# Optimization experiments

Hardware: AMD Instinct MI355X
Metric: run time of the kernel (lower is better)

The kernel has to match this reference:

```python
import jax, jax.numpy as jnp
import numpy as np

N_NODES = 50000
N_EDGES = 600000
D_FEAT = 128
HIDDEN = 128
N_CLASSES = 47


def setup_inputs() -> dict:
    key = jax.random.key(0)
    ks = jax.random.split(key, 8)
    x = jax.random.normal(ks[0], (N_NODES, D_FEAT), dtype=jnp.float32)
    edge_index = jax.random.randint(ks[1], (2, N_EDGES), 0, N_NODES, dtype=jnp.int64)
    def glorot(k, shape):
        fan_in, fan_out = shape
        s = jnp.sqrt(2.0 / (fan_in + fan_out)).astype(jnp.float32)
        return jax.random.normal(k, shape, dtype=jnp.float32) * s
    return {
        "x": x,
        "edge_index": edge_index,
        "Wl0": glorot(ks[2], (D_FEAT, HIDDEN)),
        "bl0": jnp.zeros((HIDDEN,), jnp.float32),
        "Wr0": glorot(ks[3], (D_FEAT, HIDDEN)),
        "Wl1": glorot(ks[4], (HIDDEN, HIDDEN)),
        "bl1": jnp.zeros((HIDDEN,), jnp.float32),
        "Wr1": glorot(ks[5], (HIDDEN, HIDDEN)),
        "Wl2": glorot(ks[6], (HIDDEN, N_CLASSES)),
        "bl2": jnp.zeros((N_CLASSES,), jnp.float32),
        "Wr2": glorot(ks[7], (HIDDEN, N_CLASSES)),
    }


def _sage_conv(x, src, dst, Wl, bl, Wr, n_nodes):
    # mean-aggregate neighbor (source) features at destination nodes
    msg = x[src]                                                  # [E, D] gather
    agg = jax.ops.segment_sum(msg, dst, num_segments=n_nodes)     # [N, D]
    deg = jax.ops.segment_sum(jnp.ones((src.shape[0],), x.dtype), dst,
                              num_segments=n_nodes)               # [N]
    agg = agg / jnp.maximum(deg, 1.0)[:, None]
    # PyG SAGEConv: lin_l(aggr) + lin_r(x_root); bias lives in lin_l
    return agg @ Wl + bl + x @ Wr


def reference(x, edge_index, Wl0, bl0, Wr0, Wl1, bl1, Wr1, Wl2, bl2, Wr2):
    src, dst = edge_index[0], edge_index[1]
    n = x.shape[0]
    h = jax.nn.relu(_sage_conv(x, src, dst, Wl0, bl0, Wr0, n))
    h = jax.nn.relu(_sage_conv(h, src, dst, Wl1, bl1, Wr1, n))
    h = _sage_conv(h, src, dst, Wl2, bl2, Wr2, n)
    # F.normalize(p=2, dim=-1): eps-clamped L2 norm (torch eps=1e-12)
    norm = jnp.maximum(jnp.linalg.norm(h, axis=-1, keepdims=True), 1e-12)
    h = h / norm
    return jax.nn.log_softmax(h, axis=1)
```

## Files before the change

kernel.cpp:

```cpp
#include <hip/hip_runtime.h>
#include <stdint.h>

#define N_NODES 50000
#define N_EDGES 600000
#define NCLS    47
#define SCAN_TPB 512
#define SCAN_BLOCKS ((N_NODES + SCAN_TPB - 1) / SCAN_TPB)

typedef __attribute__((ext_vector_type(8))) short short8;
typedef __attribute__((ext_vector_type(4))) float f32x4;

static __device__ __forceinline__ float bf2f(uint16_t h) {
    union { uint32_t u; float f; } c; c.u = ((uint32_t)h) << 16; return c.f;
}
static __device__ __forceinline__ float bf2fs(short h) { return bf2f((uint16_t)h); }
static __device__ __forceinline__ uint16_t f2bf(float f) {
    union { float f; uint32_t u; } c; c.f = f;
    uint32_t u = c.u;
    return (uint16_t)((u + 0x7fffu + ((u >> 16) & 1u)) >> 16);
}

__global__ __launch_bounds__(256) void k_split(const float4* __restrict__ x,
                                               ushort4* __restrict__ xh) {
    int i = blockIdx.x * 256 + threadIdx.x;
    float4 v = x[i];
    ushort4 h;
    h.x = f2bf(v.x);
    h.y = f2bf(v.y);
    h.z = f2bf(v.z);
    h.w = f2bf(v.w);
    xh[i] = h;
}

__global__ __launch_bounds__(256) void k_deg(const int* __restrict__ ei,
                                             int* __restrict__ deg) {
    __shared__ int is64;
    {
        int lane = threadIdx.x;
        if (lane < 64) {
            int f = ei[2 * lane + 1] | ei[2 * lane + 129];
            unsigned long long m = __ballot(f != 0);
            if (lane == 0) is64 = (m == 0ULL) ? 1 : 0;
        }
        __syncthreads();
    }
    int e = blockIdx.x * 256 + threadIdx.x;
    if (e < N_EDGES) {
        int d = is64 ? ei[2 * (N_EDGES + e)] : ei[N_EDGES + e];
        d = min(max(d, 0), N_NODES - 1);
        atomicAdd(&deg[d], 1);
    }
}

__global__ __launch_bounds__(SCAN_TPB) void k_scan1(const int* __restrict__ deg,
                                                    int* __restrict__ partial) {
    int t = blockIdx.x * SCAN_TPB + threadIdx.x;
    int v = (t < N_NODES) ? deg[t] : 0;
#pragma unroll
    for (int o = 1; o < 64; o <<= 1) v += __shfl_xor(v, o);
    __shared__ int ws[SCAN_TPB / 64];
    int lane = threadIdx.x & 63, w = threadIdx.x >> 6;
    if (lane == 0) ws[w] = v;
    __syncthreads();
    if (threadIdx.x == 0) {
        int s = 0;
#pragma unroll
        for (int i = 0; i < SCAN_TPB / 64; ++i) s += ws[i];
        partial[blockIdx.x] = s;
    }
}

__global__ __launch_bounds__(128) void k_scan2(int* __restrict__ partial) {
    __shared__ int sh[128];
    int t = threadIdx.x;
    int v = (t < SCAN_BLOCKS) ? partial[t] : 0;
    sh[t] = v;
    __syncthreads();
    for (int o = 1; o < 128; o <<= 1) {
        int u = (t >= o) ? sh[t - o] : 0;
        __syncthreads();
        sh[t] += u;
        __syncthreads();
    }
    if (t < SCAN_BLOCKS) partial[t] = sh[t] - v;
}

__global__ __launch_bounds__(SCAN_TPB) void k_scan3(const int* __restrict__ deg,
                                                    const int* __restrict__ partial,
                                                    int* __restrict__ row_start,
                                                    int* __restrict__ fill,
                                                    float* __restrict__ inv_deg) {
    int tb = threadIdx.x;
    int t = blockIdx.x * SCAN_TPB + tb;
    int v = (t < N_NODES) ? deg[t] : 0;
    int lane = tb & 63, w = tb >> 6;
    int inc = v;
#pragma unroll
    for (int o = 1; o < 64; o <<= 1) {
        int u = __shfl_up(inc, o);
        if (lane >= o) inc += u;
    }
    __shared__ int wsum[SCAN_TPB / 64];
    if (lane == 63) wsum[w] = inc;
    __syncthreads();
    int woff = 0;
    for (int i = 0; i < w; ++i) woff += wsum[i];
    int excl = partial[blockIdx.x] + woff + (inc - v);
    if (t < N_NODES) {
        row_start[t] = excl;
        fill[t] = excl;
        inv_deg[t] = 1.0f / (float)(v > 0 ? v : 1);
    }
}

__global__ __launch_bounds__(256) void k_fill(const int* __restrict__ ei,
                                              int* __restrict__ fill,
                                              int* __restrict__ elist) {
    __shared__ int is64;
    {
        int lane = threadIdx.x;
        if (lane < 64) {
            int f = ei[2 * lane + 1] | ei[2 * lane + 129];
            unsigned long long m = __ballot(f != 0);
            if (lane == 0) is64 = (m == 0ULL) ? 1 : 0;
        }
        __syncthreads();
    }
    int e = blockIdx.x * 256 + threadIdx.x;
    if (e < N_EDGES) {
        int s, d;
        if (is64) { s = ei[2 * e]; d = ei[2 * (N_EDGES + e)]; }
        else      { s = ei[e];     d = ei[N_EDGES + e]; }
        s = min(max(s, 0), N_NODES - 1);
        d = min(max(d, 0), N_NODES - 1);
        int pos = atomicAdd(&fill[d], 1);
        elist[pos] = s;
    }
}

__global__ __launch_bounds__(256) void k_agg(const uint16_t* __restrict__ hm_h,
                                             const int* __restrict__ row_start,
                                             const int* __restrict__ degv,
                                             const float* __restrict__ inv_deg,
                                             const int* __restrict__ elist,
                                             uint16_t* __restrict__ agg_h) {
    int lane = threadIdx.x & 63;
    int node = blockIdx.x * 4 + (threadIdx.x >> 6);
    if (node >= N_NODES) return;
    int g = lane >> 4;
    int li = lane & 15;
    int j = li * 8;
    int rs = row_start[node];
    int d = degv[node];
    float a[8];
#pragma unroll
    for (int k = 0; k < 8; ++k) a[k] = 0.f;
    int i = g;
    for (; i + 4 < d; i += 8) {
        int s0 = elist[rs + i];
        int s1 = elist[rs + i + 4];
        short8 w0 = *(const short8*)&hm_h[(size_t)s0 * 128 + j];
        short8 w1 = *(const short8*)&hm_h[(size_t)s1 * 128 + j];
#pragma unroll
        for (int k = 0; k < 8; ++k) a[k] += bf2fs(w0[k]) + bf2fs(w1[k]);
    }
    if (i < d) {
        int s = elist[rs + i];
        short8 w = *(const short8*)&hm_h[(size_t)s * 128 + j];
#pragma unroll
        for (int k = 0; k < 8; ++k) a[k] += bf2fs(w[k]);
    }
    float sc = inv_deg[node];
    short8 oh;
#pragma unroll
    for (int k = 0; k < 8; ++k) {
        float v = a[k];
        v += __shfl_xor(v, 16);
        v += __shfl_xor(v, 32);
        oh[k] = (short)f2bf(v * sc);
    }
    if (g == 0) *(short8*)&agg_h[(size_t)node * 128 + j] = oh;
}

__global__ __launch_bounds__(256) void k_prepw(const float* Wl0, const float* Wr0,
                                               const float* Wl1, const float* Wr1,
                                               const float* Wl2, const float* Wr2,
                                               uint16_t* __restrict__ img) {
    int b = blockIdx.x >> 6;
    int sub = blockIdx.x & 63;
    const float* W; int ncol, npad; uint16_t* o;
    switch (b) {
        case 0: W = Wl0; ncol = 128; npad = 128; o = img;           break;
        case 1: W = Wr0; ncol = 128; npad = 128; o = img + 32768;   break;
        case 2: W = Wl1; ncol = 128; npad = 128; o = img + 65536;   break;
        case 3: W = Wr1; ncol = 128; npad = 128; o = img + 98304;   break;
        case 4: W = Wl2; ncol = 47;  npad = 48;  o = img + 131072;  break;
        default:W = Wr2; ncol = 47;  npad = 48;  o = img + 143360;  break;
    }
    int elems = npad * 128;
    int i = sub * 256 + threadIdx.x;
    if (i < elems) {
        int col = i % npad, k = i / npad;
        float v = (col < ncol) ? W[k * ncol + col] : 0.f;
        uint16_t h = f2bf(v);
        uint16_t l = f2bf(v - bf2f(h));
        int idx = col * 128 + (((k >> 3) ^ (col & 15)) << 3) + (k & 7);
        o[idx] = h;
        o[idx + elems] = l;
    }
}

__global__ __launch_bounds__(512) void k_gemm(const uint16_t* __restrict__ A1h,
                                              const uint16_t* __restrict__ A2h,
                                              const uint16_t* __restrict__ wl,
                                              const uint16_t* __restrict__ wr,
                                              const float* __restrict__ bias,
                                              uint16_t* __restrict__ outh) {
    __shared__ __align__(16) uint16_t ldsW[32768];
    int tid = threadIdx.x;
    int lane = tid & 63, wv = tid >> 6;
    int li = lane & 15, g4 = lane >> 4;
    int mrow = blockIdx.x * 128 + wv * 16 + li;
    int r0 = min(mrow, N_NODES - 1);

    f32x4 acc[8];
#pragma unroll
    for (int t = 0; t < 8; ++t) acc[t] = (f32x4){0.f, 0.f, 0.f, 0.f};

#pragma unroll
    for (int arr = 0; arr < 2; ++arr) {
        {
            const uint4* g = (const uint4*)(arr ? wr : wl);
            uint4* l = (uint4*)ldsW;
#pragma unroll
            for (int j2 = 0; j2 < 8; ++j2)
                l[j2 * 512 + tid] = g[j2 * 512 + tid];
        }
        __syncthreads();

        const uint16_t* Ah = arr ? A2h : A1h;
#pragma unroll
        for (int s = 0; s < 4; ++s) {
            int ko = s * 32 + g4 * 8;
            short8 a0h = *(const short8*)&Ah[(size_t)r0 * 128 + ko];
#pragma unroll
            for (int t = 0; t < 8; ++t) {
                int off = (t * 16 + li) * 128 + (((s * 4 + g4) ^ li) << 3);
                short8 bh = *(const short8*)&ldsW[off];
                short8 bl = *(const short8*)&ldsW[off + 16384];
                acc[t] = __builtin_amdgcn_mfma_f32_16x16x32_bf16(a0h, bh, acc[t], 0, 0, 0);
                acc[t] = __builtin_amdgcn_mfma_f32_16x16x32_bf16(a0h, bl, acc[t], 0, 0, 0);
            }
        }
        if (arr == 0) __syncthreads();
    }
    int rowbase = blockIdx.x * 128 + wv * 16 + g4 * 4;
#pragma unroll
    for (int t = 0; t < 8; ++t) {
        int col = t * 16 + li;
        float bv = bias[col];
#pragma unroll
        for (int rr = 0; rr < 4; ++rr) {
            int row = rowbase + rr;
            if (row < N_NODES)
                outh[(size_t)row * 128 + col] = f2bf(fmaxf(acc[t][rr] + bv, 0.f));
        }
    }
}

__global__ __launch_bounds__(512) void k_gemm2(const uint16_t* __restrict__ A1h,
                                               const uint16_t* __restrict__ A2h,
                                               const uint16_t* __restrict__ w2,
                                               const float* __restrict__ bias,
                                               float* __restrict__ out) {
    __shared__ __align__(16) uint16_t ldsW[24576];
    int tid = threadIdx.x;
    int lane = tid & 63, wv = tid >> 6;
    int li = lane & 15, g4 = lane >> 4;
    int mrow = blockIdx.x * 128 + wv * 16 + li;
    int r = min(mrow, N_NODES - 1);

    {
        const uint4* g = (const uint4*)w2;
        uint4* l = (uint4*)ldsW;
#pragma unroll
        for (int j2 = 0; j2 < 12; ++j2)
            l[j2 * 512 + tid] = g[j2 * 512 + tid];
    }
    __syncthreads();

    f32x4 acc[3];
#pragma unroll
    for (int t = 0; t < 3; ++t) acc[t] = (f32x4){0.f, 0.f, 0.f, 0.f};

#pragma unroll
    for (int arr = 0; arr < 2; ++arr) {
        const uint16_t* Ah = arr ? A2h : A1h;
        const uint16_t* WL = &ldsW[arr * 12288];
#pragma unroll
        for (int s = 0; s < 4; ++s) {
            int ko = s * 32 + g4 * 8;
            short8 ah = *(const short8*)&Ah[(size_t)r * 128 + ko];
#pragma unroll
            for (int t = 0; t < 3; ++t) {
                int off = (t * 16 + li) * 128 + (((s * 4 + g4) ^ li) << 3);
                short8 bh = *(const short8*)&WL[off];
                short8 bl = *(const short8*)&WL[off + 6144];
                acc[t] = __builtin_amdgcn_mfma_f32_16x16x32_bf16(ah, bh, acc[t], 0, 0, 0);
                acc[t] = __builtin_amdgcn_mfma_f32_16x16x32_bf16(ah, bl, acc[t], 0, 0, 0);
            }
        }
    }

    float b0 = bias[li];
    float b1 = bias[16 + li];
    bool v2ok = (li < 15);
    float b2 = v2ok ? bias[32 + li] : 0.f;

    int rowbase = blockIdx.x * 128 + wv * 16 + g4 * 4;
#pragma unroll
    for (int rr = 0; rr < 4; ++rr) {
        int row = rowbase + rr;
        float v0 = acc[0][rr] + b0;
        float v1 = acc[1][rr] + b1;
        float v2 = v2ok ? (acc[2][rr] + b2) : 0.f;
        float ss = v0 * v0 + v1 * v1 + v2 * v2;
        ss += __shfl_xor(ss, 1);
        ss += __shfl_xor(ss, 2);
        ss += __shfl_xor(ss, 4);
        ss += __shfl_xor(ss, 8);
        float inv = 1.f / fmaxf(sqrtf(ss), 1e-12f);
        v0 *= inv; v1 *= inv; v2 *= inv;
        float mx = fmaxf(v0, v1);
        if (v2ok) mx = fmaxf(mx, v2);
        mx = fmaxf(mx, __shfl_xor(mx, 1));
        mx = fmaxf(mx, __shfl_xor(mx, 2));
        mx = fmaxf(mx, __shfl_xor(mx, 4));
        mx = fmaxf(mx, __shfl_xor(mx, 8));
        float se = expf(v0 - mx) + expf(v1 - mx) + (v2ok ? expf(v2 - mx) : 0.f);
        se += __shfl_xor(se, 1);
        se += __shfl_xor(se, 2);
        se += __shfl_xor(se, 4);
        se += __shfl_xor(se, 8);
        float lse = logf(se);
        if (row < N_NODES) {
            size_t ob = (size_t)row * NCLS;
            out[ob + li]      = v0 - mx - lse;
            out[ob + 16 + li] = v1 - mx - lse;
            if (v2ok) out[ob + 32 + li] = v2 - mx - lse;
        }
    }
}

extern "C" void kernel_launch(void* const* d_in, const int* in_sizes, int n_in,
                              void* d_out, int out_size, void* d_ws, size_t ws_size,
                              hipStream_t stream) {
    const float* x   = (const float*)d_in[0];
    const int*   ei  = (const int*)d_in[1];
    const float* Wl0 = (const float*)d_in[2];
    const float* bl0 = (const float*)d_in[3];
    const float* Wr0 = (const float*)d_in[4];
    const float* Wl1 = (const float*)d_in[5];
    const float* bl1 = (const float*)d_in[6];
    const float* Wr1 = (const float*)d_in[7];
    const float* Wl2 = (const float*)d_in[8];
    const float* bl2 = (const float*)d_in[9];
    const float* Wr2 = (const float*)d_in[10];
    float* out = (float*)d_out;

    char* ws = (char*)d_ws;
    size_t cur = 0;
    auto alloc = [&](size_t bytes) {
        char* p = ws + cur;
        cur += (bytes + 255) & ~(size_t)255;
        return p;
    };
    const size_t MATB = (size_t)N_NODES * 128 * 2;
    int*      deg       = (int*)alloc(N_NODES * 4);
    int*      row_start = (int*)alloc(N_NODES * 4);
    int*      fill      = (int*)alloc(N_NODES * 4);
    float*    inv_deg   = (float*)alloc(N_NODES * 4);
    int*      partial   = (int*)alloc(SCAN_BLOCKS * 4);
    int*      elist     = (int*)alloc(N_EDGES * 4);
    uint16_t* wimg      = (uint16_t*)alloc(155648 * 2);
    uint16_t* xh        = (uint16_t*)alloc(MATB);
    uint16_t* Ah        = (uint16_t*)alloc(MATB);
    uint16_t* Bh        = (uint16_t*)alloc(MATB);
    uint16_t* Ch        = (uint16_t*)alloc(MATB);

    hipMemsetAsync(deg, 0, N_NODES * 4, stream);
    k_prepw<<<384, 256, 0, stream>>>(Wl0, Wr0, Wl1, Wr1, Wl2, Wr2, wimg);
    k_split<<<(N_NODES * 128 / 4) / 256, 256, 0, stream>>>((const float4*)x, (ushort4*)xh);

    int egrid = (N_EDGES + 255) / 256;
    k_deg<<<egrid, 256, 0, stream>>>(ei, deg);
    k_scan1<<<SCAN_BLOCKS, SCAN_TPB, 0, stream>>>(deg, partial);
    k_scan2<<<1, 128, 0, stream>>>(partial);
    k_scan3<<<SCAN_BLOCKS, SCAN_TPB, 0, stream>>>(deg, partial, row_start, fill, inv_deg);
    k_fill<<<egrid, 256, 0, stream>>>(ei, fill, elist);

    int agrid = (N_NODES + 3) / 4;
    int ggrid = (N_NODES + 127) / 128;

    k_agg<<<agrid, 256, 0, stream>>>(xh, row_start, deg, inv_deg, elist, Ah);
    k_gemm<<<ggrid, 512, 0, stream>>>(Ah, xh, wimg, wimg + 32768, bl0, Bh);
    k_agg<<<agrid, 256, 0, stream>>>(Bh, row_start, deg, inv_deg, elist, Ah);
    k_gemm<<<ggrid, 512, 0, stream>>>(Ah, Bh, wimg + 65536, wimg + 98304, bl1, Ch);
    k_agg<<<agrid, 256, 0, stream>>>(Ch, row_start, deg, inv_deg, elist, Ah);
    k_gemm2<<<ggrid, 512, 0, stream>>>(Ah, Ch, wimg + 131072, bl2, out);
}
```

Baseline: 287.6 us.

## Fuse neighbor mean aggregation into the SAGE GEMM kernels

Removes the standalone k_agg kernel and the intermediate aggregated buffer. Each GEMM lane now gathers its own row's neighbors and builds the mean directly as its MFMA A operand, which drops three launches and the write and re-read of a 50000x128 bf16 matrix per layer. The cost is much less gather parallelism: only 391 blocks, one row per 4-lane group, two edges in flight per lane, and divergence from differing degrees within a wave. The added register pressure under launch_bounds(512,4) may also cause spills.

```diff
diff --git a/kernel.cpp b/kernel.cpp
--- a/kernel.cpp
+++ b/kernel.cpp
@@ -136,50 +136,6 @@
         int pos = atomicAdd(&fill[d], 1);
         elist[pos] = s;
     }
-}
-
-__global__ __launch_bounds__(256) void k_agg(const uint16_t* __restrict__ hm_h,
-                                             const int* __restrict__ row_start,
-                                             const int* __restrict__ degv,
-                                             const float* __restrict__ inv_deg,
-                                             const int* __restrict__ elist,
-                                             uint16_t* __restrict__ agg_h) {
-    int lane = threadIdx.x & 63;
-    int node = blockIdx.x * 4 + (threadIdx.x >> 6);
-    if (node >= N_NODES) return;
-    int g = lane >> 4;
-    int li = lane & 15;
-    int j = li * 8;
-    int rs = row_start[node];
-    int d = degv[node];
-    float a[8];
-#pragma unroll
-    for (int k = 0; k < 8; ++k) a[k] = 0.f;
-    int i = g;
-    for (; i + 4 < d; i += 8) {
-        int s0 = elist[rs + i];
-        int s1 = elist[rs + i + 4];
-        short8 w0 = *(const short8*)&hm_h[(size_t)s0 * 128 + j];
-        short8 w1 = *(const short8*)&hm_h[(size_t)s1 * 128 + j];
-#pragma unroll
-        for (int k = 0; k < 8; ++k) a[k] += bf2fs(w0[k]) + bf2fs(w1[k]);
-    }
-    if (i < d) {
-        int s = elist[rs + i];
-        short8 w = *(const short8*)&hm_h[(size_t)s * 128 + j];
-#pragma unroll
-        for (int k = 0; k < 8; ++k) a[k] += bf2fs(w[k]);
-    }
-    float sc = inv_deg[node];
-    short8 oh;
-#pragma unroll
-    for (int k = 0; k < 8; ++k) {
-        float v = a[k];
-        v += __shfl_xor(v, 16);
-        v += __shfl_xor(v, 32);
-        oh[k] = (short)f2bf(v * sc);
-    }
-    if (g == 0) *(short8*)&agg_h[(size_t)node * 128 + j] = oh;
 }
 
 __global__ __launch_bounds__(256) void k_prepw(const float* Wl0, const float* Wr0,
@@ -210,12 +166,15 @@
     }
 }
 
-__global__ __launch_bounds__(512) void k_gemm(const uint16_t* __restrict__ A1h,
-                                              const uint16_t* __restrict__ A2h,
-                                              const uint16_t* __restrict__ wl,
-                                              const uint16_t* __restrict__ wr,
-                                              const float* __restrict__ bias,
-                                              uint16_t* __restrict__ outh) {
+__global__ __launch_bounds__(512, 4) void k_gemm(const uint16_t* __restrict__ Ain,
+                                                 const int* __restrict__ row_start,
+                                                 const int* __restrict__ degv,
+                                                 const float* __restrict__ inv_deg,
+                                                 const int* __restrict__ elist,
+                                                 const uint16_t* __restrict__ wl,
+                                                 const uint16_t* __restrict__ wr,
+                                                 const float* __restrict__ bias,
+                                                 uint16_t* __restrict__ outh) {
     __shared__ __align__(16) uint16_t ldsW[32768];
     int tid = threadIdx.x;
     int lane = tid & 63, wv = tid >> 6;
@@ -223,6 +182,62 @@
     int mrow = blockIdx.x * 128 + wv * 16 + li;
     int r0 = min(mrow, N_NODES - 1);
 
+    float ag[4][8];
+#pragma unroll
+    for (int s = 0; s < 4; ++s)
+#pragma unroll
+        for (int k = 0; k < 8; ++k) ag[s][k] = 0.f;
+    {
+        int rs = row_start[r0];
+        int d = degv[r0];
+        int i = 0;
+        for (; i + 1 < d; i += 2) {
+            int n0 = elist[rs + i];
+            int n1 = elist[rs + i + 1];
+            const uint16_t* p0 = &Ain[(size_t)n0 * 128 + g4 * 8];
+            const uint16_t* p1 = &Ain[(size_t)n1 * 128 + g4 * 8];
+            short8 u0 = *(const short8*)&p0[0];
+            short8 u1 = *(const short8*)&p0[32];
+            short8 u2 = *(const short8*)&p0[64];
+            short8 u3 = *(const short8*)&p0[96];
+            short8 v0 = *(const short8*)&p1[0];
+            short8 v1 = *(const short8*)&p1[32];
+            short8 v2 = *(const short8*)&p1[64];
+            short8 v3 = *(const short8*)&p1[96];
+#pragma unroll
+            for (int k = 0; k < 8; ++k) {
+                ag[0][k] += bf2fs(u0[k]) + bf2fs(v0[k]);
+                ag[1][k] += bf2fs(u1[k]) + bf2fs(v1[k]);
+                ag[2][k] += bf2fs(u2[k]) + bf2fs(v2[k]);
+                ag[3][k] += bf2fs(u3[k]) + bf2fs(v3[k]);
+            }
+        }
+        if (i < d) {
+            int n0 = elist[rs + i];
+            const uint16_t* p0 = &Ain[(size_t)n0 * 128 + g4 * 8];
+            short8 u0 = *(const short8*)&p0[0];
+            short8 u1 = *(const short8*)&p0[32];
+            short8 u2 = *(const short8*)&p0[64];
+            short8 u3 = *(const short8*)&p0[96];
+#pragma unroll
+            for (int k = 0; k < 8; ++k) {
+                ag[0][k] += bf2fs(u0[k]);
+                ag[1][k] += bf2fs(u1[k]);
+                ag[2][k] += bf2fs(u2[k]);
+                ag[3][k] += bf2fs(u3[k]);
+            }
+        }
+    }
+    short8 a1[4];
+    {
+        float sc = inv_deg[r0];
+#pragma unroll
+        for (int s = 0; s < 4; ++s)
+#pragma unroll
+            for (int k = 0; k < 8; ++k)
+                a1[s][k] = (short)f2bf(ag[s][k] * sc);
+    }
+
     f32x4 acc[8];
 #pragma unroll
     for (int t = 0; t < 8; ++t) acc[t] = (f32x4){0.f, 0.f, 0.f, 0.f};
@@ -237,19 +252,18 @@
                 l[j2 * 512 + tid] = g[j2 * 512 + tid];
         }
         __syncthreads();
-
-        const uint16_t* Ah = arr ? A2h : A1h;
 #pragma unroll
         for (int s = 0; s < 4; ++s) {
-            int ko = s * 32 + g4 * 8;
-            short8 a0h = *(const short8*)&Ah[(size_t)r0 * 128 + ko];
+            short8 av;
+            if (arr == 0) av = a1[s];
+            else av = *(const short8*)&Ain[(size_t)r0 * 128 + s * 32 + g4 * 8];
 #pragma unroll
             for (int t = 0; t < 8; ++t) {
                 int off = (t * 16 + li) * 128 + (((s * 4 + g4) ^ li) << 3);
                 short8 bh = *(const short8*)&ldsW[off];
                 short8 bl = *(const short8*)&ldsW[off + 16384];
-                acc[t] = __builtin_amdgcn_mfma_f32_16x16x32_bf16(a0h, bh, acc[t], 0, 0, 0);
-                acc[t] = __builtin_amdgcn_mfma_f32_16x16x32_bf16(a0h, bl, acc[t], 0, 0, 0);
+                acc[t] = __builtin_amdgcn_mfma_f32_16x16x32_bf16(av, bh, acc[t], 0, 0, 0);
+                acc[t] = __builtin_amdgcn_mfma_f32_16x16x32_bf16(av, bl, acc[t], 0, 0, 0);
             }
         }
         if (arr == 0) __syncthreads();
@@ -268,11 +282,14 @@
     }
 }
 
-__global__ __launch_bounds__(512) void k_gemm2(const uint16_t* __restrict__ A1h,
-                                               const uint16_t* __restrict__ A2h,
-                                               const uint16_t* __restrict__ w2,
-                                               const float* __restrict__ bias,
-                                               float* __restrict__ out) {
+__global__ __launch_bounds__(512, 4) void k_gemm2(const uint16_t* __restrict__ Ain,
+                                                  const int* __restrict__ row_start,
+                                                  const int* __restrict__ degv,
+                                                  const float* __restrict__ inv_deg,
+                                                  const int* __restrict__ elist,
+                                                  const uint16_t* __restrict__ w2,
+                                                  const float* __restrict__ bias,
+                                                  float* __restrict__ out) {
     __shared__ __align__(16) uint16_t ldsW[24576];
     int tid = threadIdx.x;
     int lane = tid & 63, wv = tid >> 6;
@@ -287,6 +304,62 @@
         for (int j2 = 0; j2 < 12; ++j2)
             l[j2 * 512 + tid] = g[j2 * 512 + tid];
     }
+
+    float ag[4][8];
+#pragma unroll
+    for (int s = 0; s < 4; ++s)
+#pragma unroll
+        for (int k = 0; k < 8; ++k) ag[s][k] = 0.f;
+    {
+        int rs = row_start[r];
+        int d = degv[r];
+        int i = 0;
+        for (; i + 1 < d; i += 2) {
+            int n0 = elist[rs + i];
+            int n1 = elist[rs + i + 1];
+            const uint16_t* p0 = &Ain[(size_t)n0 * 128 + g4 * 8];
+            const uint16_t* p1 = &Ain[(size_t)n1 * 128 + g4 * 8];
+            short8 u0 = *(const short8*)&p0[0];
+            short8 u1 = *(const short8*)&p0[32];
+            short8 u2 = *(const short8*)&p0[64];
+            short8 u3 = *(const short8*)&p0[96];
+            short8 v0 = *(const short8*)&p1[0];
+            short8 v1 = *(const short8*)&p1[32];
+            short8 v2 = *(const short8*)&p1[64];
+            short8 v3 = *(const short8*)&p1[96];
+#pragma unroll
+            for (int k = 0; k < 8; ++k) {
+                ag[0][k] += bf2fs(u0[k]) + bf2fs(v0[k]);
+                ag[1][k] += bf2fs(u1[k]) + bf2fs(v1[k]);
+                ag[2][k] += bf2fs(u2[k]) + bf2fs(v2[k]);
+                ag[3][k] += bf2fs(u3[k]) + bf2fs(v3[k]);
+            }
+        }
+        if (i < d) {
+            int n0 = elist[rs + i];
+            const uint16_t* p0 = &Ain[(size_t)n0 * 128 + g4 * 8];
+            short8 u0 = *(const short8*)&p0[0];
+            short8 u1 = *(const short8*)&p0[32];
+            short8 u2 = *(const short8*)&p0[64];
+            short8 u3 = *(const short8*)&p0[96];
+#pragma unroll
+            for (int k = 0; k < 8; ++k) {
+                ag[0][k] += bf2fs(u0[k]);
+                ag[1][k] += bf2fs(u1[k]);
+                ag[2][k] += bf2fs(u2[k]);
+                ag[3][k] += bf2fs(u3[k]);
+            }
+        }
+    }
+    short8 a1[4];
+    {
+        float sc = inv_deg[r];
+#pragma unroll
+        for (int s = 0; s < 4; ++s)
+#pragma unroll
+            for (int k = 0; k < 8; ++k)
+                a1[s][k] = (short)f2bf(ag[s][k] * sc);
+    }
     __syncthreads();
 
     f32x4 acc[3];
@@ -295,19 +368,19 @@
 
 #pragma unroll
     for (int arr = 0; arr < 2; ++arr) {
-        const uint16_t* Ah = arr ? A2h : A1h;
         const uint16_t* WL = &ldsW[arr * 12288];
 #pragma unroll
         for (int s = 0; s < 4; ++s) {
-            int ko = s * 32 + g4 * 8;
-            short8 ah = *(const short8*)&Ah[(size_t)r * 128 + ko];
+            short8 av;
+            if (arr == 0) av = a1[s];
+            else av = *(const short8*)&Ain[(size_t)r * 128 + s * 32 + g4 * 8];
 #pragma unroll
             for (int t = 0; t < 3; ++t) {
                 int off = (t * 16 + li) * 128 + (((s * 4 + g4) ^ li) << 3);
                 short8 bh = *(const short8*)&WL[off];
                 short8 bl = *(const short8*)&WL[off + 6144];
-                acc[t] = __builtin_amdgcn_mfma_f32_16x16x32_bf16(ah, bh, acc[t], 0, 0, 0);
-                acc[t] = __builtin_amdgcn_mfma_f32_16x16x32_bf16(ah, bl, acc[t], 0, 0, 0);
+                acc[t] = __builtin_amdgcn_mfma_f32_16x16x32_bf16(av, bh, acc[t], 0, 0, 0);
+                acc[t] = __builtin_amdgcn_mfma_f32_16x16x32_bf16(av, bl, acc[t], 0, 0, 0);
             }
         }
     }
@@ -384,7 +457,6 @@
     int*      elist     = (int*)alloc(N_EDGES * 4);
     uint16_t* wimg      = (uint16_t*)alloc(155648 * 2);
     uint16_t* xh        = (uint16_t*)alloc(MATB);
-    uint16_t* Ah        = (uint16_t*)alloc(MATB);
     uint16_t* Bh        = (uint16_t*)alloc(MATB);
     uint16_t* Ch        = (uint16_t*)alloc(MATB);
 
@@ -399,13 +471,12 @@
     k_scan3<<<SCAN_BLOCKS, SCAN_TPB, 0, stream>>>(deg, partial, row_start, fill, inv_deg);
     k_fill<<<egrid, 256, 0, stream>>>(ei, fill, elist);
 
-    int agrid = (N_NODES + 3) / 4;
     int ggrid = (N_NODES + 127) / 128;
 
-    k_agg<<<agrid, 256, 0, stream>>>(xh, row_start, deg, inv_deg, elist, Ah);
-    k_gemm<<<ggrid, 512, 0, stream>>>(Ah, xh, wimg, wimg + 32768, bl0, Bh);
-    k_agg<<<agrid, 256, 0, stream>>>(Bh, row_start, deg, inv_deg, elist, Ah);
-    k_gemm<<<ggrid, 512, 0, stream>>>(Ah, Bh, wimg + 65536, wimg + 98304, bl1, Ch);
-    k_agg<<<agrid, 256, 0, stream>>>(Ch, row_start, deg, inv_deg, elist, Ah);
-    k_gemm2<<<ggrid, 512, 0, stream>>>(Ah, Ch, wimg + 131072, bl2, out);
-}
+    k_gemm<<<ggrid, 512, 0, stream>>>(xh, row_start, deg, inv_deg, elist,
+                                      wimg, wimg + 32768, bl0, Bh);
+    k_gemm<<<ggrid, 512, 0, stream>>>(Bh, row_start, deg, inv_deg, elist,
+                                      wimg + 65536, wimg + 98304, bl1, Ch);
+    k_gemm2<<<ggrid, 512, 0, stream>>>(Ch, row_start, deg, inv_deg, elist,
+                                       wimg + 131072, bl2, out);
+}
```

New measurement: 291.6 us. No clear change (+1.4%).
